# Performance work log

Measured on AMD Instinct MI355X. Metric: run time of the kernel, lower is better.

The kernel has to match this reference:

```python
import jax, jax.numpy as jnp
import numpy as np

NUM_HEADS = 16


def setup_inputs() -> dict:
    key = jax.random.key(0)
    ks = jax.random.split(key, 10)
    B, C, T, K, E = 2, 4, 512, 1024, 1024
    s = 0.02
    return {
        "hidden_states": jax.random.normal(ks[0], (B, T, E), jnp.float32),
        "key_value_states": jax.random.normal(ks[1], (B, C, K, E), jnp.float32),
        "Wq": jax.random.normal(ks[2], (E, E), jnp.float32) * s,
        "bq": jax.random.normal(ks[3], (E,), jnp.float32) * s,
        "Wk": jax.random.normal(ks[4], (E, E), jnp.float32) * s,
        "bk": jax.random.normal(ks[5], (E,), jnp.float32) * s,
        "Wv": jax.random.normal(ks[6], (E, E), jnp.float32) * s,
        "bv": jax.random.normal(ks[7], (E,), jnp.float32) * s,
        "Wo": jax.random.normal(ks[8], (E, E), jnp.float32) * s,
        "bo": jax.random.normal(ks[9], (E,), jnp.float32) * s,
    }


def reference(hidden_states, key_value_states, Wq, bq, Wk, bk, Wv, bv, Wo, bo):
    B, C, K, E = key_value_states.shape
    T = hidden_states.shape[1]
    H = NUM_HEADS
    Dh = E // H
    scaling = Dh ** (-0.5)
    # q: [B,H,T,Dh]
    q = ((hidden_states @ Wq.T + bq) * scaling).reshape(B, T, H, Dh).transpose(0, 2, 1, 3)
    # k, v: [B,H,K,C,Dh]  (matches torch view(B,C,K,H,Dh).transpose(1,3))
    k = (key_value_states @ Wk.T + bk).reshape(B, C, K, H, Dh).transpose(0, 3, 2, 1, 4)
    v = (key_value_states @ Wv.T + bv).reshape(B, C, K, H, Dh).transpose(0, 3, 2, 1, 4)
    # scores: [B,H,T,K,C]; softmax over kv_len axis (per channel)
    scores = jnp.einsum("bhtd,bhkcd->bhtkc", q, k)
    probs = jax.nn.softmax(scores, axis=3)
    # default channel pooling weight = 1/C (channel_weight=None path)
    cw = jnp.full((B, C), 1.0 / C, dtype=probs.dtype)
    # attend + weighted channel-sum -> [B,T,H,Dh] -> [B,T,E]
    attn = jnp.einsum("bhtkc,bhkcd,bc->bthd", probs, v, cw).reshape(B, T, E)
    return attn @ Wo.T + bo
```

## Files before the change

kernel.cpp:

```cpp
#include <hip/hip_runtime.h>
#include <hip/hip_bf16.h>

#define DIM_B 2
#define DIM_C 4
#define DIM_T 512
#define DIM_K 1024
#define DIM_E 1024
#define DIM_H 16
#define DIM_DH 64

typedef __attribute__((ext_vector_type(8))) short bf16x8;
typedef __attribute__((ext_vector_type(4))) short bf16x4;
typedef __attribute__((ext_vector_type(4))) float f32x4;

#define MFMA_BF16(a, b, c) __builtin_amdgcn_mfma_f32_16x16x32_bf16((a), (b), (c), 0, 0, 0)

static __device__ __forceinline__ short f2bf(float f) {
    union { float f; unsigned u; } v; v.f = f;
    unsigned r = v.u + 0x7fffu + ((v.u >> 16) & 1u);
    return (short)(r >> 16);
}

static __device__ __forceinline__ void gload16(const short* g, short* lds) {
    __builtin_amdgcn_global_load_lds(
        (const __attribute__((address_space(1))) unsigned int*)g,
        (__attribute__((address_space(3))) unsigned int*)lds, 16, 0, 0);
}

__global__ __launch_bounds__(256) void cast6(
    const float* __restrict__ kvs, const float* __restrict__ hs,
    const float* __restrict__ wq, const float* __restrict__ wk,
    const float* __restrict__ wv, const float* __restrict__ wo,
    short* kvsb, short* hsb, short* wqb, short* wkb, short* wvb, short* wob)
{
    int blk = blockIdx.x;
    const float* src; short* dst; size_t off;
    if (blk < 4096) { src = kvs; dst = kvsb; off = (size_t)blk * 2048; }
    else {
        int s = (blk - 4096) >> 9;
        off = (size_t)((blk - 4096) & 511) * 2048;
        switch (s) {
            case 0: src = hs; dst = hsb; break;
            case 1: src = wq; dst = wqb; break;
            case 2: src = wk; dst = wkb; break;
            case 3: src = wv; dst = wvb; break;
            default: src = wo; dst = wob; break;
        }
    }
    size_t i = off + (size_t)threadIdx.x * 8;
    float4 a = *(const float4*)(src + i);
    float4 b = *(const float4*)(src + i + 4);
    bf16x8 o;
    o[0] = f2bf(a.x); o[1] = f2bf(a.y); o[2] = f2bf(a.z); o[3] = f2bf(a.w);
    o[4] = f2bf(b.x); o[5] = f2bf(b.y); o[6] = f2bf(b.z); o[7] = f2bf(b.w);
    *(bf16x8*)(dst + i) = o;
}

template <bool A_BF16, bool OUT_BF16, bool BIAS_ROW>
static __device__ __forceinline__ void gemm_tile(
    const void* __restrict__ Av, const short* __restrict__ W,
    const float* __restrict__ bias, void* __restrict__ Ov,
    int N, int Kd, float scale, int bm, int bn, short* As, short* Bs)
{
    const int tid = threadIdx.x;
    const int wave = tid >> 6, lane = tid & 63;
    const int L = lane & 15, Q = lane >> 4;
    const int wm = (wave & 1) * 64, wn = (wave >> 1) * 64;
    const int lr = lane >> 3;
    const int lc = ((lane & 7) ^ lr) * 8;

    f32x4 acc[4][4] = {};

    for (int k0 = 0; k0 < Kd; k0 += 64) {
        __syncthreads();
        if (A_BF16) {
            const short* A = (const short*)Av;
#pragma unroll
            for (int i = 0; i < 4; ++i) {
                int r = wave * 32 + i * 8;
                gload16(A + (size_t)(bm + r + lr) * Kd + k0 + lc, As + r * 64);
            }
        } else {
            const float* A = (const float*)Av;
#pragma unroll
            for (int rep = 0; rep < 4; ++rep) {
                int row = (tid >> 3) + rep * 32;
                int p = tid & 7;
                const float* src = A + (size_t)(bm + row) * Kd + k0 + p * 8;
                float4 a = *(const float4*)src;
                float4 b = *(const float4*)(src + 4);
                bf16x8 o;
                o[0] = f2bf(a.x); o[1] = f2bf(a.y); o[2] = f2bf(a.z); o[3] = f2bf(a.w);
                o[4] = f2bf(b.x); o[5] = f2bf(b.y); o[6] = f2bf(b.z); o[7] = f2bf(b.w);
                *(bf16x8*)&As[row * 64 + ((p ^ (row & 7)) * 8)] = o;
            }
        }
#pragma unroll
        for (int i = 0; i < 4; ++i) {
            int r = wave * 32 + i * 8;
            gload16(W + (size_t)(bn + r + lr) * Kd + k0 + lc, Bs + r * 64);
        }
        __syncthreads();
#pragma unroll
        for (int s = 0; s < 2; ++s) {
            bf16x8 af[4], bfr[4];
#pragma unroll
            for (int i = 0; i < 4; ++i)
                af[i] = *(const bf16x8*)&As[(wm + i * 16 + L) * 64 + (((s * 4 + Q) ^ (L & 7)) * 8)];
#pragma unroll
            for (int j = 0; j < 4; ++j)
                bfr[j] = *(const bf16x8*)&Bs[(wn + j * 16 + L) * 64 + (((s * 4 + Q) ^ (L & 7)) * 8)];
#pragma unroll
            for (int i = 0; i < 4; ++i)
#pragma unroll
                for (int j = 0; j < 4; ++j)
                    acc[i][j] = MFMA_BF16(af[i], bfr[j], acc[i][j]);
        }
    }

#pragma unroll
    for (int i = 0; i < 4; ++i) {
        int row0 = bm + wm + i * 16 + Q * 4;
#pragma unroll
        for (int j = 0; j < 4; ++j) {
            int col = bn + wn + j * 16 + L;
            float bj = BIAS_ROW ? 0.f : bias[col];
#pragma unroll
            for (int r = 0; r < 4; ++r) {
                float bb = BIAS_ROW ? bias[row0 + r] : bj;
                float o = (acc[i][j][r] + bb) * scale;
                if (OUT_BF16)
                    ((short*)Ov)[(size_t)(row0 + r) * N + col] = f2bf(o);
                else
                    ((float*)Ov)[(size_t)(row0 + r) * N + col] = o;
            }
        }
    }
}

template <bool A_BF16, bool OUT_BF16>
static __device__ __forceinline__ void gemm_tile64(
    const void* __restrict__ Av, const short* __restrict__ W,
    const float* __restrict__ bias, void* __restrict__ Ov,
    int N, int Kd, float scale, int bm, int bn, short* As, short* Bs)
{
    const int tid = threadIdx.x;
    const int wave = tid >> 6, lane = tid & 63;
    const int L = lane & 15, Q = lane >> 4;
    const int wm = (wave & 1) * 32, wn = (wave >> 1) * 32;
    const int lr = lane >> 3;
    const int lc = ((lane & 7) ^ lr) * 8;

    f32x4 acc[2][2] = {};

    for (int k0 = 0; k0 < Kd; k0 += 64) {
        __syncthreads();
        if (A_BF16) {
            const short* A = (const short*)Av;
#pragma unroll
            for (int i = 0; i < 2; ++i) {
                int r = wave * 16 + i * 8;
                gload16(A + (size_t)(bm + r + lr) * Kd + k0 + lc, As + r * 64);
            }
        } else {
            const float* A = (const float*)Av;
#pragma unroll
            for (int rep = 0; rep < 2; ++rep) {
                int row = (tid >> 3) + rep * 32;
                int p = tid & 7;
                const float* src = A + (size_t)(bm + row) * Kd + k0 + p * 8;
                float4 a = *(const float4*)src;
                float4 b = *(const float4*)(src + 4);
                bf16x8 o;
                o[0] = f2bf(a.x); o[1] = f2bf(a.y); o[2] = f2bf(a.z); o[3] = f2bf(a.w);
                o[4] = f2bf(b.x); o[5] = f2bf(b.y); o[6] = f2bf(b.z); o[7] = f2bf(b.w);
                *(bf16x8*)&As[row * 64 + ((p ^ (row & 7)) * 8)] = o;
            }
        }
#pragma unroll
        for (int i = 0; i < 2; ++i) {
            int r = wave * 16 + i * 8;
            gload16(W + (size_t)(bn + r + lr) * Kd + k0 + lc, Bs + r * 64);
        }
        __syncthreads();
#pragma unroll
        for (int s = 0; s < 2; ++s) {
            bf16x8 af[2], bfr[2];
#pragma unroll
            for (int i = 0; i < 2; ++i)
                af[i] = *(const bf16x8*)&As[(wm + i * 16 + L) * 64 + (((s * 4 + Q) ^ (L & 7)) * 8)];
#pragma unroll
            for (int j = 0; j < 2; ++j)
                bfr[j] = *(const bf16x8*)&Bs[(wn + j * 16 + L) * 64 + (((s * 4 + Q) ^ (L & 7)) * 8)];
#pragma unroll
            for (int i = 0; i < 2; ++i)
#pragma unroll
                for (int j = 0; j < 2; ++j)
                    acc[i][j] = MFMA_BF16(af[i], bfr[j], acc[i][j]);
        }
    }

#pragma unroll
    for (int i = 0; i < 2; ++i) {
        int row0 = bm + wm + i * 16 + Q * 4;
#pragma unroll
        for (int j = 0; j < 2; ++j) {
            int col = bn + wn + j * 16 + L;
            float bj = bias[col];
#pragma unroll
            for (int r = 0; r < 4; ++r) {
                float o = (acc[i][j][r] + bj) * scale;
                if (OUT_BF16)
                    ((short*)Ov)[(size_t)(row0 + r) * N + col] = f2bf(o);
                else
                    ((float*)Ov)[(size_t)(row0 + r) * N + col] = o;
            }
        }
    }
}

__global__ __launch_bounds__(256) void gemm_qkv(
    const short* __restrict__ hsb, const short* __restrict__ wqb,
    const float* __restrict__ bq, short* __restrict__ qb,
    const short* __restrict__ kvsb, const short* __restrict__ wkb,
    const float* __restrict__ bk, short* __restrict__ kb,
    const short* __restrict__ wvb, const float* __restrict__ bv,
    short* __restrict__ vtb)
{
    __shared__ alignas(16) short As[128 * 64];
    __shared__ alignas(16) short Bs[128 * 64];
    int blk = blockIdx.x;
    if (blk < 256) {
        int i = blk;
        int bm = (i & 7) + 8 * (i >> 7);
        int bn = (i >> 3) & 15;
        gemm_tile64<true, true>(hsb, wqb, bq, qb, DIM_E, DIM_E, 0.125f,
                                bm * 64, bn * 64, As, Bs);
    } else if (blk < 768) {
        int i = blk - 256;
        int bm = (i & 7) + 8 * (i >> 6);
        int bn = (i >> 3) & 7;
        gemm_tile<true, true, false>(kvsb, wkb, bk, kb, DIM_E, DIM_E, 1.0f,
                                     bm * 128, bn * 128, As, Bs);
    } else {
        int i = blk - 768;
        int bn = (i & 7) + 8 * (i >> 6);
        int bm = (i >> 3) & 7;
        gemm_tile<true, true, true>(wvb, kvsb, bv, vtb, DIM_B * DIM_C * DIM_K, DIM_E, 1.0f,
                                    bm * 128, bn * 128, As, Bs);
    }
}

__global__ __launch_bounds__(256) void gemm_o(
    const float* __restrict__ A, const short* __restrict__ W,
    const float* __restrict__ bias, float* __restrict__ Out)
{
    __shared__ alignas(16) short As[64 * 64];
    __shared__ alignas(16) short Bs[64 * 64];
    int i = blockIdx.x;
    int bm = (i & 7) + 8 * (i >> 7);
    int bn = (i >> 3) & 15;
    gemm_tile64<false, false>(A, W, bias, Out, DIM_E, DIM_E, 1.0f,
                              bm * 64, bn * 64, As, Bs);
}

__global__ __launch_bounds__(256) void attn_kernel(
    const short* __restrict__ q, const short* __restrict__ k,
    const short* __restrict__ vt, float* __restrict__ attn)
{
    __shared__ alignas(16) short Ks[64 * 64];
    __shared__ alignas(16) short Vs[64 * 64];
    __shared__ alignas(16) short Pl[4][16][72];

    const int tid = threadIdx.x;
    const int wave = tid >> 6, lane = tid & 63;
    const int L = lane & 15, Q = lane >> 4;
    const int lr = lane >> 3;
    const int lc = ((lane & 7) ^ lr) * 8;
    const int x = blockIdx.x;
    const int c = x & 3, tt = (x >> 2) & 7, h = (x >> 5) & 15, b = x >> 9;
    const int t0 = tt * 64;
    const int NKV = DIM_B * DIM_C * DIM_K;

    const size_t qrow = (size_t)(b * DIM_T + t0 + wave * 16 + L) * DIM_E + h * DIM_DH;
    const bf16x8 aq0 = *(const bf16x8*)(q + qrow + Q * 8);
    const bf16x8 aq1 = *(const bf16x8*)(q + qrow + 32 + Q * 8);

    const size_t kbase = (size_t)((b * DIM_C + c) * DIM_K) * DIM_E + h * DIM_DH;
    const size_t vbase = (size_t)(h * DIM_DH) * NKV + (b * DIM_C + c) * DIM_K;

    float lsum[4] = {0.f, 0.f, 0.f, 0.f};
    f32x4 oacc[4] = {};

    const int xs0 = (Q ^ (L & 7)) * 8;
    const int xs1 = ((4 + Q) ^ (L & 7)) * 8;

    for (int kc = 0; kc < 16; ++kc) {
        const int kk0 = kc * 64;
        __syncthreads();
#pragma unroll
        for (int i = 0; i < 2; ++i) {
            int r = wave * 16 + i * 8;
            gload16(k + kbase + (size_t)(kk0 + r + lr) * DIM_E + lc, Ks + r * 64);
        }
#pragma unroll
        for (int i = 0; i < 2; ++i) {
            int r = wave * 16 + i * 8;
            gload16(vt + vbase + (size_t)(r + lr) * NKV + kk0 + lc, Vs + r * 64);
        }
        __syncthreads();
        f32x4 s4[4];
#pragma unroll
        for (int j = 0; j < 4; ++j) {
            bf16x8 bk0 = *(const bf16x8*)&Ks[(j * 16 + L) * 64 + xs0];
            bf16x8 bk1 = *(const bf16x8*)&Ks[(j * 16 + L) * 64 + xs1];
            f32x4 z = {};
            z = MFMA_BF16(aq0, bk0, z);
            s4[j] = MFMA_BF16(aq1, bk1, z);
        }
#pragma unroll
        for (int j = 0; j < 4; ++j)
#pragma unroll
            for (int r = 0; r < 4; ++r) {
                float p = __expf(s4[j][r]);
                lsum[r] += p;
                Pl[wave][Q * 4 + r][j * 16 + L] = f2bf(p);
            }
        bf16x8 ap0 = *(const bf16x8*)&Pl[wave][L][Q * 8];
        bf16x8 ap1 = *(const bf16x8*)&Pl[wave][L][32 + Q * 8];
#pragma unroll
        for (int dt = 0; dt < 4; ++dt) {
            bf16x8 bv0 = *(const bf16x8*)&Vs[(dt * 16 + L) * 64 + xs0];
            bf16x8 bv1 = *(const bf16x8*)&Vs[(dt * 16 + L) * 64 + xs1];
            oacc[dt] = MFMA_BF16(ap0, bv0, oacc[dt]);
            oacc[dt] = MFMA_BF16(ap1, bv1, oacc[dt]);
        }
    }

    float l[4];
#pragma unroll
    for (int r = 0; r < 4; ++r) {
        float t = lsum[r];
#pragma unroll
        for (int msk = 1; msk < 16; msk <<= 1)
            t += __shfl_xor(t, msk, 16);
        l[r] = t;
    }

#pragma unroll
    for (int dt = 0; dt < 4; ++dt)
#pragma unroll
        for (int r = 0; r < 4; ++r) {
            int t = t0 + wave * 16 + Q * 4 + r;
            int d = dt * 16 + L;
            atomicAdd(&attn[(size_t)(b * DIM_T + t) * DIM_E + h * DIM_DH + d],
                      oacc[dt][r] / l[r] * 0.25f);
        }
}

extern "C" void kernel_launch(void* const* d_in, const int* in_sizes, int n_in,
                              void* d_out, int out_size, void* d_ws, size_t ws_size,
                              hipStream_t stream)
{
    const float* hs  = (const float*)d_in[0];
    const float* kvs = (const float*)d_in[1];
    const float* Wq  = (const float*)d_in[2];
    const float* bq  = (const float*)d_in[3];
    const float* Wk  = (const float*)d_in[4];
    const float* bk  = (const float*)d_in[5];
    const float* Wv  = (const float*)d_in[6];
    const float* bv  = (const float*)d_in[7];
    const float* Wo  = (const float*)d_in[8];
    const float* bo  = (const float*)d_in[9];
    float* out = (float*)d_out;

    char* ws = (char*)d_ws;
    short* kvsb = (short*)(ws);
    short* hsb  = (short*)(ws + (16ull << 20));
    short* wqb  = (short*)(ws + (18ull << 20));
    short* wkb  = (short*)(ws + (20ull << 20));
    short* wvb  = (short*)(ws + (22ull << 20));
    short* wob  = (short*)(ws + (24ull << 20));
    short* qb   = (short*)(ws + (26ull << 20));
    short* kb   = (short*)(ws + (28ull << 20));
    short* vtb  = (short*)(ws + (44ull << 20));
    float* ab   = (float*)(ws + (16ull << 20));

    dim3 blk(256);
    const int MQ = DIM_B * DIM_T;

    cast6<<<dim3(4096 + 5 * 512), blk, 0, stream>>>(
        kvs, hs, Wq, Wk, Wv, Wo, kvsb, hsb, wqb, wkb, wvb, wob);

    gemm_qkv<<<dim3(256 + 512 + 512), blk, 0, stream>>>(
        hsb, wqb, bq, qb, kvsb, wkb, bk, kb, wvb, bv, vtb);

    (void)hipMemsetAsync(ab, 0, (size_t)MQ * DIM_E * sizeof(float), stream);

    attn_kernel<<<dim3(DIM_B * DIM_H * 8 * DIM_C), blk, 0, stream>>>(qb, kb, vtb, ab);

    gemm_o<<<dim3(256), blk, 0, stream>>>(ab, wob, bo, out);
}
```

Measured before the change: 214.2 us.

## Transpose score MFMA to pack probabilities and reorder attention block mapping

The QK^T MFMA operands are swapped so each lane holds four consecutive key positions for one query row. The exponentiated probabilities can then be packed into bf16 pairs with truncation and written to LDS as one 8-byte store instead of sixteen scalar stores. The row-sum reduction shrinks to two cross-quad shuffles plus broadcasts, and the divide becomes a reciprocal multiply. The block index mapping now places batch and channel in the low bits, which changes which blocks run together and contend on the atomics. Truncating instead of rounding when converting to bf16 slightly changes numerics.

```diff
diff --git a/kernel.cpp b/kernel.cpp
--- a/kernel.cpp
+++ b/kernel.cpp
@@ -12,6 +12,7 @@
 typedef __attribute__((ext_vector_type(8))) short bf16x8;
 typedef __attribute__((ext_vector_type(4))) short bf16x4;
 typedef __attribute__((ext_vector_type(4))) float f32x4;
+typedef __attribute__((ext_vector_type(2))) unsigned int u32x2;
 
 #define MFMA_BF16(a, b, c) __builtin_amdgcn_mfma_f32_16x16x32_bf16((a), (b), (c), 0, 0, 0)
 
@@ -19,6 +20,11 @@
     union { float f; unsigned u; } v; v.f = f;
     unsigned r = v.u + 0x7fffu + ((v.u >> 16) & 1u);
     return (short)(r >> 16);
+}
+
+static __device__ __forceinline__ unsigned pack_bf2(float lo, float hi) {
+    union { float f; unsigned u; } a, b; a.f = lo; b.f = hi;
+    return (a.u >> 16) | (b.u & 0xffff0000u);
 }
 
 static __device__ __forceinline__ void gload16(const short* g, short* lds) {
@@ -278,7 +284,10 @@
     const int lr = lane >> 3;
     const int lc = ((lane & 7) ^ lr) * 8;
     const int x = blockIdx.x;
-    const int c = x & 3, tt = (x >> 2) & 7, h = (x >> 5) & 15, b = x >> 9;
+    const int low = x & 7;
+    const int c = low & 3, b = low >> 2;
+    const int y = x >> 3;
+    const int tt = y & 7, h = y >> 3;
     const int t0 = tt * 64;
     const int NKV = DIM_B * DIM_C * DIM_K;
 
@@ -289,7 +298,7 @@
     const size_t kbase = (size_t)((b * DIM_C + c) * DIM_K) * DIM_E + h * DIM_DH;
     const size_t vbase = (size_t)(h * DIM_DH) * NKV + (b * DIM_C + c) * DIM_K;
 
-    float lsum[4] = {0.f, 0.f, 0.f, 0.f};
+    float lsum = 0.f;
     f32x4 oacc[4] = {};
 
     const int xs0 = (Q ^ (L & 7)) * 8;
@@ -315,17 +324,19 @@
             bf16x8 bk0 = *(const bf16x8*)&Ks[(j * 16 + L) * 64 + xs0];
             bf16x8 bk1 = *(const bf16x8*)&Ks[(j * 16 + L) * 64 + xs1];
             f32x4 z = {};
-            z = MFMA_BF16(aq0, bk0, z);
-            s4[j] = MFMA_BF16(aq1, bk1, z);
-        }
-#pragma unroll
-        for (int j = 0; j < 4; ++j)
-#pragma unroll
-            for (int r = 0; r < 4; ++r) {
-                float p = __expf(s4[j][r]);
-                lsum[r] += p;
-                Pl[wave][Q * 4 + r][j * 16 + L] = f2bf(p);
-            }
+            z = MFMA_BF16(bk0, aq0, z);
+            s4[j] = MFMA_BF16(bk1, aq1, z);
+        }
+#pragma unroll
+        for (int j = 0; j < 4; ++j) {
+            float p0 = __expf(s4[j][0]), p1 = __expf(s4[j][1]);
+            float p2 = __expf(s4[j][2]), p3 = __expf(s4[j][3]);
+            lsum += (p0 + p1) + (p2 + p3);
+            u32x2 w;
+            w[0] = pack_bf2(p0, p1);
+            w[1] = pack_bf2(p2, p3);
+            *(u32x2*)&Pl[wave][L][j * 16 + Q * 4] = w;
+        }
         bf16x8 ap0 = *(const bf16x8*)&Pl[wave][L][Q * 8];
         bf16x8 ap1 = *(const bf16x8*)&Pl[wave][L][32 + Q * 8];
 #pragma unroll
@@ -337,15 +348,13 @@
         }
     }
 
-    float l[4];
-#pragma unroll
-    for (int r = 0; r < 4; ++r) {
-        float t = lsum[r];
-#pragma unroll
-        for (int msk = 1; msk < 16; msk <<= 1)
-            t += __shfl_xor(t, msk, 16);
-        l[r] = t;
-    }
+    float lr_ = lsum;
+    lr_ += __shfl_xor(lr_, 16);
+    lr_ += __shfl_xor(lr_, 32);
+    float linv[4];
+#pragma unroll
+    for (int r = 0; r < 4; ++r)
+        linv[r] = 0.25f / __shfl(lr_, Q * 4 + r);
 
 #pragma unroll
     for (int dt = 0; dt < 4; ++dt)
@@ -354,7 +363,7 @@
             int t = t0 + wave * 16 + Q * 4 + r;
             int d = dt * 16 + L;
             atomicAdd(&attn[(size_t)(b * DIM_T + t) * DIM_E + h * DIM_DH + d],
-                      oacc[dt][r] / l[r] * 0.25f);
+                      oacc[dt][r] * linv[r]);
         }
 }
 
```

New measurement: 211.1 us. No clear change (-1.4%).
